# Kernel tuning notes

Hardware: AMD Instinct MI355X
Metric: run time of the kernel (lower is better)

Reference implementation:

```python
import jax, jax.numpy as jnp
from jax import lax
import numpy as np

B, T, F = 256, 2048, 12
EV_VOCAB, RS_VOCAB = 32, 8
EED, RED = 6, 3
H, K = 96, 3
D = F + EED + RED  # 21


def setup_inputs() -> dict:
    key = jax.random.key(0)
    ks = jax.random.split(key, 12)
    s = 0.05
    return {
        'seq': jax.random.normal(ks[0], (B, T, F), jnp.float32),
        'ev': jax.random.randint(ks[1], (B, T), 0, EV_VOCAB),
        'rs': jax.random.randint(ks[2], (B, T), 0, RS_VOCAB),
        'lengths': jax.random.randint(ks[3], (B,), 1, T + 1),  # valid lengths in [1, T]
        'event_emb': jax.random.normal(ks[4], (EV_VOCAB, EED), jnp.float32) * s,
        'result_emb': jax.random.normal(ks[5], (RS_VOCAB, RED), jnp.float32) * s,
        'W_ih': jax.random.normal(ks[6], (4 * H, D), jnp.float32) * s,
        'W_hh': jax.random.normal(ks[7], (4 * H, H), jnp.float32) * s,
        'b_ih': jnp.zeros((4 * H,), jnp.float32),
        'b_hh': jnp.zeros((4 * H,), jnp.float32),
        'W_mlp': jax.random.normal(ks[8], (H, H * K), jnp.float32) * s,
        'b_mlp': jnp.zeros((H,), jnp.float32),
        'W_fc': jax.random.normal(ks[9], (2, 2 * H), jnp.float32) * s,
        'b_fc': jnp.zeros((2,), jnp.float32),
    }


def reference(seq, ev, rs, lengths, event_emb, result_emb, W_ih, W_hh, b_ih, b_hh,
              W_mlp, b_mlp, W_fc, b_fc):
    # embed + concat -> [B,T,D]
    x = jnp.concatenate([seq, event_emb[ev], result_emb[rs]], axis=-1)
    xs = jnp.swapaxes(x, 0, 1)  # [T,B,D]
    ts = jnp.arange(T)
    b = b_ih + b_hh

    def step(carry, inp):
        h, c = carry
        x_t, t = inp
        gates = x_t @ W_ih.T + h @ W_hh.T + b  # [B,4H]
        i, f, g, o = jnp.split(gates, 4, axis=-1)  # PyTorch gate order i,f,g,o
        i = jax.nn.sigmoid(i); f = jax.nn.sigmoid(f)
        g = jnp.tanh(g); o = jax.nn.sigmoid(o)
        c_new = f * c + i * g
        h_new = o * jnp.tanh(c_new)
        m = (t < lengths)[:, None]  # packed-seq semantics: freeze state past length
        h = jnp.where(m, h_new, h)
        c = jnp.where(m, c_new, c)
        out = jnp.where(m, h_new, jnp.zeros_like(h_new))  # pad_packed zeros
        return (h, c), out

    h0 = jnp.zeros((B, H), x.dtype)
    (h_fin, _), outs = lax.scan(step, (h0, h0), (xs, ts))
    out_padded = jnp.swapaxes(outs, 0, 1)  # [B,T,H]

    # vectorized last-k gather (replaces torch Python loop)
    idx = lengths[:, None] - K + jnp.arange(K)  # [B,K]
    valid = idx >= 0
    gathered = jnp.take_along_axis(out_padded, jnp.clip(idx, 0)[:, :, None], axis=1)
    gathered = jnp.where(valid[:, :, None], gathered, jnp.zeros_like(gathered))
    lastk = gathered.reshape(B, K * H)

    h_lastk = jax.nn.relu(lastk @ W_mlp.T + b_mlp)
    h = jnp.concatenate([h_fin, h_lastk], axis=1)  # [B,2H]
    return h @ W_fc.T + b_fc  # [B,2]
```

## Files before the change

kernel.cpp:

```cpp
#include <hip/hip_runtime.h>

#define TT 2048
#define FF 12
#define HH 96
#define CH 128
#define L2E 1.44269504088896340736f

__device__ __forceinline__ float fast_exp2(float x){ return __builtin_amdgcn_exp2f(x); }
__device__ __forceinline__ float fast_rcp(float x){ return __builtin_amdgcn_rcpf(x); }

__global__ __launch_bounds__(512, 2) void lstm_persist(
  const float* __restrict__ seq, const int* __restrict__ ev, const int* __restrict__ rsi,
  const int* __restrict__ len, const float* __restrict__ eemb, const float* __restrict__ remb,
  const float* __restrict__ W_ih, const float* __restrict__ W_hh,
  const float* __restrict__ b_ih, const float* __restrict__ b_hh,
  const float* __restrict__ W_mlp, const float* __restrict__ b_mlp,
  const float* __restrict__ W_fc, const float* __restrict__ b_fc,
  float* __restrict__ out)
{
  const int b   = blockIdx.x;
  const int tid = threadIdx.x;
  const int w   = tid >> 6;
  const int l   = tid & 63;

  __shared__ __align__(16) float vh[HH];
  __shared__ __align__(16) float xch[CH][32];
  __shared__ __align__(16) float part[6*8*64];
  __shared__ __align__(16) float act[384];
  __shared__ __align__(16) float lastk[3*HH];
  __shared__ __align__(16) float h2[2*HH];
  __shared__ __align__(16) float et[32*6];
  __shared__ __align__(16) float rt[8*3];
  __shared__ int evb[CH];
  __shared__ int rsb[CH];

  float wreg[96];
  if (w < 6) {
    #pragma unroll
    for (int k = 0; k < 6; ++k) {
      const int g = l + 64*k;
      const float* p = W_hh + g*96 + 16*w;
      #pragma unroll
      for (int i = 0; i < 16; ++i) wreg[k*16+i] = p[i];
    }
  } else if (w == 6) {
    #pragma unroll
    for (int k = 0; k < 6; ++k) {
      const int g = l + 64*k;
      const float* p = W_ih + g*21;
      #pragma unroll
      for (int i = 0; i < 16; ++i) wreg[k*16+i] = p[i];
    }
  } else {
    #pragma unroll
    for (int k = 0; k < 6; ++k) {
      const int g = l + 64*k;
      #pragma unroll
      for (int i = 0; i < 16; ++i) {
        const int c = 16 + i;
        wreg[k*16+i] = (c < 21) ? W_ih[g*21 + c] : 0.f;
      }
    }
  }
  const float bg = (tid < 384) ? (b_ih[tid] + b_hh[tid]) : 0.f;

  for (int i = tid; i < HH;   i += 512) vh[i] = 0.f;
  for (int i = tid; i < 3*HH; i += 512) lastk[i] = 0.f;
  for (int i = tid; i < 192;  i += 512) et[i] = eemb[i];
  for (int i = tid; i < 24;   i += 512) rt[i] = remb[i];

  float c_state = 0.f;
  const int L = len[b];

  for (int t0 = 0; t0 < L; t0 += CH) {
    for (int q = tid; q < CH*FF; q += 512) {
      const int r = q / 12;
      const int c = q - r*12;
      xch[r][c] = seq[(size_t)b*(TT*FF) + (size_t)t0*FF + q];
    }
    if (tid < CH) {
      evb[tid] = ev [b*TT + t0 + tid];
      rsb[tid] = rsi[b*TT + t0 + tid];
    }
    __syncthreads();
    for (int q = tid; q < CH*20; q += 512) {
      const int r  = q / 20;
      const int cc = q - r*20 + 12;
      float val;
      if (cc < 18)      val = et[evb[r]*6 + (cc-12)];
      else if (cc < 21) val = rt[rsb[r]*3 + (cc-18)];
      else              val = 0.f;
      xch[r][cc] = val;
    }
    __syncthreads();

    const int nr = min(CH, L - t0);
    for (int r = 0; r < nr; ++r) {
      const float* sp = (w < 6) ? (vh + 16*w) : (&xch[r][16*(w-6)]);
      const float4 q0 = ((const float4*)sp)[0];
      const float4 q1 = ((const float4*)sp)[1];
      const float4 q2 = ((const float4*)sp)[2];
      const float4 q3 = ((const float4*)sp)[3];
      const float xv[16] = {q0.x,q0.y,q0.z,q0.w, q1.x,q1.y,q1.z,q1.w,
                            q2.x,q2.y,q2.z,q2.w, q3.x,q3.y,q3.z,q3.w};
      #pragma unroll
      for (int k = 0; k < 6; ++k) {
        float a = 0.f;
        #pragma unroll
        for (int i = 0; i < 16; ++i) a = fmaf(wreg[k*16+i], xv[i], a);
        part[(k*8 + w)*64 + l] = a;
      }
      __syncthreads();
      if (tid < 384) {
        float s = bg;
        const int kk = tid >> 6;
        const int ll = tid & 63;
        #pragma unroll
        for (int ww = 0; ww < 8; ++ww) s += part[(kk*8 + ww)*64 + ll];
        const bool is_t = (tid >= 192) && (tid < 288);
        const float arg = is_t ? (-2.f*L2E)*fabsf(s) : (-L2E)*s;
        const float e  = fast_exp2(arg);
        const float r1 = fast_rcp(1.f + e);
        const float th = copysignf((1.f - e) * r1, s);
        act[tid] = is_t ? th : r1;
      }
      __syncthreads();
      if (tid < 96) {
        const float i_ = act[tid];
        const float f_ = act[96  + tid];
        const float g_ = act[192 + tid];
        const float o_ = act[288 + tid];
        c_state = fmaf(f_, c_state, i_*g_);
        const float e  = fast_exp2((-2.f*L2E)*fabsf(c_state));
        const float th = copysignf((1.f - e) * fast_rcp(1.f + e), c_state);
        const float hn = o_ * th;
        vh[tid] = hn;
        const int kk = (t0 + r) + 3 - L;
        if (kk >= 0) lastk[kk*96 + tid] = hn;
      }
      __syncthreads();
    }
  }

  if (tid < 192) {
    const int hh = tid / 96;
    const int m  = tid - hh*96;
    const float* wp = W_mlp + m*288 + hh*144;
    const float* xp = lastk + hh*144;
    float s = 0.f;
    #pragma unroll 8
    for (int i = 0; i < 144; ++i) s = fmaf(wp[i], xp[i], s);
    act[tid] = s;
  }
  __syncthreads();
  if (tid < 96) {
    const float hl = act[tid] + act[96+tid] + b_mlp[tid];
    h2[96 + tid] = fmaxf(hl, 0.f);
    h2[tid] = vh[tid];
  }
  __syncthreads();
  if (tid < 128) {
    const int o  = tid >> 6;
    const int ll = tid & 63;
    const float* wf = W_fc + o*192 + 3*ll;
    float s = fmaf(wf[0], h2[3*ll+0], fmaf(wf[1], h2[3*ll+1], wf[2]*h2[3*ll+2]));
    #pragma unroll
    for (int off = 32; off > 0; off >>= 1) s += __shfl_down(s, off);
    if (ll == 0) out[b*2 + o] = s + b_fc[o];
  }
}

extern "C" void kernel_launch(void* const* d_in, const int* in_sizes, int n_in,
                              void* d_out, int out_size, void* d_ws, size_t ws_size,
                              hipStream_t stream) {
  const float* seq   = (const float*)d_in[0];
  const int*   ev    = (const int*)  d_in[1];
  const int*   rsi   = (const int*)  d_in[2];
  const int*   len   = (const int*)  d_in[3];
  const float* eemb  = (const float*)d_in[4];
  const float* remb  = (const float*)d_in[5];
  const float* W_ih  = (const float*)d_in[6];
  const float* W_hh  = (const float*)d_in[7];
  const float* b_ih  = (const float*)d_in[8];
  const float* b_hh  = (const float*)d_in[9];
  const float* W_mlp = (const float*)d_in[10];
  const float* b_mlp = (const float*)d_in[11];
  const float* W_fc  = (const float*)d_in[12];
  const float* b_fc  = (const float*)d_in[13];

  hipLaunchKernelGGL(lstm_persist, dim3(256), dim3(512), 0, stream,
                     seq, ev, rsi, len, eemb, remb, W_ih, W_hh, b_ih, b_hh,
                     W_mlp, b_mlp, W_fc, b_fc, (float*)d_out);
}
```

Baseline: 1.329 ms.

## Restructure LSTM step: per-thread gate rows, shuffle gate exchange, one barrier per step

Each of 384 threads now owns one full gate row, holding all of W_hh and W_ih in registers, so the cross-wave partial-sum reduction through shared memory goes away. The four gates of a hidden unit sit in adjacent lanes and are combined with xor shuffles. The hidden state is double-buffered, so each timestep needs one barrier instead of three. The input projection for the next step is computed ahead, and packed 2-wide FMAs are used for the recurrent dot product. The cost is much higher register pressure (about 117 weight registers per thread) and a serial 96-long dot product per thread on the critical path.

```diff
diff --git a/kernel.cpp b/kernel.cpp
--- a/kernel.cpp
+++ b/kernel.cpp
@@ -2,14 +2,17 @@
 
 #define TT 2048
 #define FF 12
-#define HH 96
 #define CH 128
 #define L2E 1.44269504088896340736f
 
+typedef float v2f __attribute__((ext_vector_type(2)));
+
 __device__ __forceinline__ float fast_exp2(float x){ return __builtin_amdgcn_exp2f(x); }
 __device__ __forceinline__ float fast_rcp(float x){ return __builtin_amdgcn_rcpf(x); }
+__device__ __forceinline__ v2f fma2(v2f a, v2f b, v2f c){ return __builtin_elementwise_fma(a, b, c); }
+__device__ __forceinline__ v2f mk2(float x, float y){ v2f r; r.x = x; r.y = y; return r; }
 
-__global__ __launch_bounds__(512, 2) void lstm_persist(
+__global__ __launch_bounds__(384, 2) void lstm_persist(
   const float* __restrict__ seq, const int* __restrict__ ev, const int* __restrict__ rsi,
   const int* __restrict__ len, const float* __restrict__ eemb, const float* __restrict__ remb,
   const float* __restrict__ W_ih, const float* __restrict__ W_hh,
@@ -20,143 +23,142 @@
 {
   const int b   = blockIdx.x;
   const int tid = threadIdx.x;
-  const int w   = tid >> 6;
-  const int l   = tid & 63;
+  const int qg  = tid & 3;
+  const int u   = tid >> 2;
+  const int g   = qg*96 + u;
 
-  __shared__ __align__(16) float vh[HH];
-  __shared__ __align__(16) float xch[CH][32];
-  __shared__ __align__(16) float part[6*8*64];
-  __shared__ __align__(16) float act[384];
-  __shared__ __align__(16) float lastk[3*HH];
-  __shared__ __align__(16) float h2[2*HH];
-  __shared__ __align__(16) float et[32*6];
-  __shared__ __align__(16) float rt[8*3];
+  __shared__ __align__(16) float xf[CH*24];
+  __shared__ __align__(16) float vhbuf[2*96];
+  __shared__ __align__(16) float lastk[3*96];
+  __shared__ __align__(16) float et[192];
+  __shared__ __align__(16) float rt[24];
+  __shared__ __align__(16) float accs[192];
+  __shared__ __align__(16) float h2[2*96];
   __shared__ int evb[CH];
   __shared__ int rsb[CH];
 
-  float wreg[96];
-  if (w < 6) {
+  v2f wh[48];
+  {
+    const float4* wp = (const float4*)(W_hh + g*96);
     #pragma unroll
-    for (int k = 0; k < 6; ++k) {
-      const int g = l + 64*k;
-      const float* p = W_hh + g*96 + 16*w;
-      #pragma unroll
-      for (int i = 0; i < 16; ++i) wreg[k*16+i] = p[i];
-    }
-  } else if (w == 6) {
-    #pragma unroll
-    for (int k = 0; k < 6; ++k) {
-      const int g = l + 64*k;
-      const float* p = W_ih + g*21;
-      #pragma unroll
-      for (int i = 0; i < 16; ++i) wreg[k*16+i] = p[i];
-    }
-  } else {
-    #pragma unroll
-    for (int k = 0; k < 6; ++k) {
-      const int g = l + 64*k;
-      #pragma unroll
-      for (int i = 0; i < 16; ++i) {
-        const int c = 16 + i;
-        wreg[k*16+i] = (c < 21) ? W_ih[g*21 + c] : 0.f;
-      }
+    for (int k = 0; k < 24; ++k) {
+      const float4 q4 = wp[k];
+      wh[2*k]   = mk2(q4.x, q4.y);
+      wh[2*k+1] = mk2(q4.z, q4.w);
     }
   }
-  const float bg = (tid < 384) ? (b_ih[tid] + b_hh[tid]) : 0.f;
+  float wi[21];
+  #pragma unroll
+  for (int c = 0; c < 21; ++c) wi[c] = W_ih[g*21 + c];
+  const float bg = b_ih[g] + b_hh[g];
 
-  for (int i = tid; i < HH;   i += 512) vh[i] = 0.f;
-  for (int i = tid; i < 3*HH; i += 512) lastk[i] = 0.f;
-  for (int i = tid; i < 192;  i += 512) et[i] = eemb[i];
-  for (int i = tid; i < 24;   i += 512) rt[i] = remb[i];
+  if (tid < 192) { vhbuf[tid] = 0.f; et[tid] = eemb[tid]; }
+  if (tid < 24)  rt[tid] = remb[tid];
+  if (tid < 288) lastk[tid] = 0.f;
 
   float c_state = 0.f;
   const int L = len[b];
 
   for (int t0 = 0; t0 < L; t0 += CH) {
-    for (int q = tid; q < CH*FF; q += 512) {
-      const int r = q / 12;
-      const int c = q - r*12;
-      xch[r][c] = seq[(size_t)b*(TT*FF) + (size_t)t0*FF + q];
+    #pragma unroll
+    for (int qq = 0; qq < 4; ++qq) {
+      const int i = tid + qq*384;
+      const int r = i/12, c = i - r*12;
+      xf[r*24 + c] = seq[(size_t)b*(TT*FF) + (size_t)t0*FF + i];
     }
     if (tid < CH) {
       evb[tid] = ev [b*TT + t0 + tid];
       rsb[tid] = rsi[b*TT + t0 + tid];
     }
     __syncthreads();
-    for (int q = tid; q < CH*20; q += 512) {
-      const int r  = q / 20;
-      const int cc = q - r*20 + 12;
-      float val;
-      if (cc < 18)      val = et[evb[r]*6 + (cc-12)];
-      else if (cc < 21) val = rt[rsb[r]*3 + (cc-18)];
-      else              val = 0.f;
-      xch[r][cc] = val;
+    #pragma unroll
+    for (int qq = 0; qq < 4; ++qq) {
+      const int i = tid + qq*384;
+      const int r = i/12, cc = i - r*12 + 12;
+      float v;
+      if (cc < 18)      v = et[evb[r]*6 + (cc-12)];
+      else if (cc < 21) v = rt[rsb[r]*3 + (cc-18)];
+      else              v = 0.f;
+      xf[r*24 + cc] = v;
     }
     __syncthreads();
 
     const int nr = min(CH, L - t0);
+    float xp;
+    {
+      const float* xr = xf;
+      float s0 = bg, s1 = 0.f, s2 = 0.f;
+      #pragma unroll
+      for (int c = 0; c < 7; ++c) {
+        s0 = fmaf(wi[c],    xr[c],    s0);
+        s1 = fmaf(wi[c+7],  xr[c+7],  s1);
+        s2 = fmaf(wi[c+14], xr[c+14], s2);
+      }
+      xp = s0 + s1 + s2;
+    }
+
     for (int r = 0; r < nr; ++r) {
-      const float* sp = (w < 6) ? (vh + 16*w) : (&xch[r][16*(w-6)]);
-      const float4 q0 = ((const float4*)sp)[0];
-      const float4 q1 = ((const float4*)sp)[1];
-      const float4 q2 = ((const float4*)sp)[2];
-      const float4 q3 = ((const float4*)sp)[3];
-      const float xv[16] = {q0.x,q0.y,q0.z,q0.w, q1.x,q1.y,q1.z,q1.w,
-                            q2.x,q2.y,q2.z,q2.w, q3.x,q3.y,q3.z,q3.w};
+      const float4* hq = (const float4*)(vhbuf + (r&1)*96);
+      v2f a0 = mk2(xp, 0.f), a1 = mk2(0.f,0.f), a2 = mk2(0.f,0.f), a3 = mk2(0.f,0.f);
       #pragma unroll
-      for (int k = 0; k < 6; ++k) {
-        float a = 0.f;
+      for (int k = 0; k < 24; k += 2) {
+        const float4 h4 = hq[k];
+        const float4 h5 = hq[k+1];
+        a0 = fma2(wh[2*k],   mk2(h4.x,h4.y), a0);
+        a1 = fma2(wh[2*k+1], mk2(h4.z,h4.w), a1);
+        a2 = fma2(wh[2*k+2], mk2(h5.x,h5.y), a2);
+        a3 = fma2(wh[2*k+3], mk2(h5.z,h5.w), a3);
+      }
+      const float s = ((a0.x+a0.y)+(a1.x+a1.y)) + ((a2.x+a2.y)+(a3.x+a3.y));
+      const bool is_t = (qg == 2);
+      const float arg = is_t ? (-2.f*L2E)*fabsf(s) : (-L2E)*s;
+      const float e  = fast_exp2(arg);
+      const float r1 = fast_rcp(1.f + e);
+      const float th = copysignf((1.f - e)*r1, s);
+      const float a  = is_t ? th : r1;
+      const float t1 = __shfl_xor(a, 2);
+      const float t2 = __shfl_xor(a, 1);
+      const float t3 = __shfl_xor(t1, 1);
+      if (qg == 0) {
+        c_state = fmaf(t2, c_state, a*t1);
+        const float e2  = fast_exp2((-2.f*L2E)*fabsf(c_state));
+        const float th2 = copysignf((1.f - e2)*fast_rcp(1.f + e2), c_state);
+        const float hn  = t3 * th2;
+        vhbuf[((r&1)^1)*96 + u] = hn;
+        const int kk = (t0 + r) + 3 - L;
+        if (kk >= 0) lastk[kk*96 + u] = hn;
+      }
+      if (r + 1 < nr) {
+        const float* xr = xf + (r+1)*24;
+        float s0 = bg, s1 = 0.f, s2 = 0.f;
         #pragma unroll
-        for (int i = 0; i < 16; ++i) a = fmaf(wreg[k*16+i], xv[i], a);
-        part[(k*8 + w)*64 + l] = a;
-      }
-      __syncthreads();
-      if (tid < 384) {
-        float s = bg;
-        const int kk = tid >> 6;
-        const int ll = tid & 63;
-        #pragma unroll
-        for (int ww = 0; ww < 8; ++ww) s += part[(kk*8 + ww)*64 + ll];
-        const bool is_t = (tid >= 192) && (tid < 288);
-        const float arg = is_t ? (-2.f*L2E)*fabsf(s) : (-L2E)*s;
-        const float e  = fast_exp2(arg);
-        const float r1 = fast_rcp(1.f + e);
-        const float th = copysignf((1.f - e) * r1, s);
-        act[tid] = is_t ? th : r1;
-      }
-      __syncthreads();
-      if (tid < 96) {
-        const float i_ = act[tid];
-        const float f_ = act[96  + tid];
-        const float g_ = act[192 + tid];
-        const float o_ = act[288 + tid];
-        c_state = fmaf(f_, c_state, i_*g_);
-        const float e  = fast_exp2((-2.f*L2E)*fabsf(c_state));
-        const float th = copysignf((1.f - e) * fast_rcp(1.f + e), c_state);
-        const float hn = o_ * th;
-        vh[tid] = hn;
-        const int kk = (t0 + r) + 3 - L;
-        if (kk >= 0) lastk[kk*96 + tid] = hn;
+        for (int c = 0; c < 7; ++c) {
+          s0 = fmaf(wi[c],    xr[c],    s0);
+          s1 = fmaf(wi[c+7],  xr[c+7],  s1);
+          s2 = fmaf(wi[c+14], xr[c+14], s2);
+        }
+        xp = s0 + s1 + s2;
       }
       __syncthreads();
     }
   }
 
+  const float* hf = vhbuf + (L & 1)*96;
   if (tid < 192) {
-    const int hh = tid / 96;
-    const int m  = tid - hh*96;
-    const float* wp = W_mlp + m*288 + hh*144;
-    const float* xp = lastk + hh*144;
+    const int half = tid / 96;
+    const int m    = tid - half*96;
+    const float* wp = W_mlp + m*288 + half*144;
+    const float* xq = lastk + half*144;
     float s = 0.f;
     #pragma unroll 8
-    for (int i = 0; i < 144; ++i) s = fmaf(wp[i], xp[i], s);
-    act[tid] = s;
+    for (int i = 0; i < 144; ++i) s = fmaf(wp[i], xq[i], s);
+    accs[tid] = s;
   }
   __syncthreads();
   if (tid < 96) {
-    const float hl = act[tid] + act[96+tid] + b_mlp[tid];
+    const float hl = accs[tid] + accs[96+tid] + b_mlp[tid];
     h2[96 + tid] = fmaxf(hl, 0.f);
-    h2[tid] = vh[tid];
+    h2[tid] = hf[tid];
   }
   __syncthreads();
   if (tid < 128) {
@@ -188,7 +190,7 @@
   const float* W_fc  = (const float*)d_in[12];
   const float* b_fc  = (const float*)d_in[13];
 
-  hipLaunchKernelGGL(lstm_persist, dim3(256), dim3(512), 0, stream,
+  hipLaunchKernelGGL(lstm_persist, dim3(256), dim3(384), 0, stream,
                      seq, ev, rsi, len, eemb, remb, W_ih, W_hh, b_ih, b_hh,
                      W_mlp, b_mlp, W_fc, b_fc, (float*)d_out);
 }
```

Measured after the change: 1.468 ms. 1.1x slower.

## Fuse gate activation and cell update via lane shuffles, use packed FMA

Applied to the files above, without the earlier changes.

Remaps the gate-reduction threads so each group of four adjacent lanes holds the i, f, g, o gates of one hidden unit. Shuffles then exchange the activations and the cell update runs in the same phase, which removes one block-wide barrier and the shared-memory act round trip per timestep. The per-step matvec now uses packed two-wide FMA on paired weight registers with split accumulators, and the partial-sum buffer is padded to a stride of 66. The cost is scattered reads of the partial sums and only a quarter of the lanes doing the cell update.

```diff
diff --git a/kernel.cpp b/kernel.cpp
--- a/kernel.cpp
+++ b/kernel.cpp
@@ -4,10 +4,15 @@
 #define FF 12
 #define HH 96
 #define CH 128
+#define PST 66
 #define L2E 1.44269504088896340736f
+
+typedef float v2f __attribute__((ext_vector_type(2)));
 
 __device__ __forceinline__ float fast_exp2(float x){ return __builtin_amdgcn_exp2f(x); }
 __device__ __forceinline__ float fast_rcp(float x){ return __builtin_amdgcn_rcpf(x); }
+__device__ __forceinline__ v2f fma2(v2f a, v2f b, v2f c){ return __builtin_elementwise_fma(a, b, c); }
+__device__ __forceinline__ v2f mk2(float x, float y){ v2f r; r.x = x; r.y = y; return r; }
 
 __global__ __launch_bounds__(512, 2) void lstm_persist(
   const float* __restrict__ seq, const int* __restrict__ ev, const int* __restrict__ rsi,
@@ -25,23 +30,23 @@
 
   __shared__ __align__(16) float vh[HH];
   __shared__ __align__(16) float xch[CH][32];
-  __shared__ __align__(16) float part[6*8*64];
-  __shared__ __align__(16) float act[384];
+  __shared__ __align__(16) float part[6*8*PST];
   __shared__ __align__(16) float lastk[3*HH];
   __shared__ __align__(16) float h2[2*HH];
+  __shared__ __align__(16) float accs[192];
   __shared__ __align__(16) float et[32*6];
   __shared__ __align__(16) float rt[8*3];
   __shared__ int evb[CH];
   __shared__ int rsb[CH];
 
-  float wreg[96];
+  v2f wreg[48];
   if (w < 6) {
     #pragma unroll
     for (int k = 0; k < 6; ++k) {
       const int g = l + 64*k;
       const float* p = W_hh + g*96 + 16*w;
       #pragma unroll
-      for (int i = 0; i < 16; ++i) wreg[k*16+i] = p[i];
+      for (int i = 0; i < 8; ++i) wreg[k*8+i] = mk2(p[2*i], p[2*i+1]);
     }
   } else if (w == 6) {
     #pragma unroll
@@ -49,20 +54,28 @@
       const int g = l + 64*k;
       const float* p = W_ih + g*21;
       #pragma unroll
-      for (int i = 0; i < 16; ++i) wreg[k*16+i] = p[i];
+      for (int i = 0; i < 8; ++i) wreg[k*8+i] = mk2(p[2*i], p[2*i+1]);
     }
   } else {
     #pragma unroll
     for (int k = 0; k < 6; ++k) {
       const int g = l + 64*k;
       #pragma unroll
-      for (int i = 0; i < 16; ++i) {
-        const int c = 16 + i;
-        wreg[k*16+i] = (c < 21) ? W_ih[g*21 + c] : 0.f;
+      for (int i = 0; i < 8; ++i) {
+        const int c0 = 16 + 2*i, c1 = 17 + 2*i;
+        const float w0 = (c0 < 21) ? W_ih[g*21 + c0] : 0.f;
+        const float w1 = (c1 < 21) ? W_ih[g*21 + c1] : 0.f;
+        wreg[k*8+i] = mk2(w0, w1);
       }
     }
   }
-  const float bg = (tid < 384) ? (b_ih[tid] + b_hh[tid]) : 0.f;
+
+  const int ub = tid >> 2;
+  const int qb = tid & 3;
+  const int gb = qb*96 + ub;
+  const float bg = (tid < 384) ? (b_ih[gb] + b_hh[gb]) : 0.f;
+  const int pk_ = gb >> 6;
+  const int pl_ = gb & 63;
 
   for (int i = tid; i < HH;   i += 512) vh[i] = 0.f;
   for (int i = tid; i < 3*HH; i += 512) lastk[i] = 0.f;
@@ -101,42 +114,47 @@
       const float4 q1 = ((const float4*)sp)[1];
       const float4 q2 = ((const float4*)sp)[2];
       const float4 q3 = ((const float4*)sp)[3];
-      const float xv[16] = {q0.x,q0.y,q0.z,q0.w, q1.x,q1.y,q1.z,q1.w,
-                            q2.x,q2.y,q2.z,q2.w, q3.x,q3.y,q3.z,q3.w};
+      v2f xv[8];
+      xv[0] = mk2(q0.x,q0.y); xv[1] = mk2(q0.z,q0.w);
+      xv[2] = mk2(q1.x,q1.y); xv[3] = mk2(q1.z,q1.w);
+      xv[4] = mk2(q2.x,q2.y); xv[5] = mk2(q2.z,q2.w);
+      xv[6] = mk2(q3.x,q3.y); xv[7] = mk2(q3.z,q3.w);
       #pragma unroll
       for (int k = 0; k < 6; ++k) {
-        float a = 0.f;
-        #pragma unroll
-        for (int i = 0; i < 16; ++i) a = fmaf(wreg[k*16+i], xv[i], a);
-        part[(k*8 + w)*64 + l] = a;
+        v2f a0 = mk2(0.f,0.f), a1 = mk2(0.f,0.f), a2 = mk2(0.f,0.f), a3 = mk2(0.f,0.f);
+        a0 = fma2(wreg[k*8+0], xv[0], a0);
+        a1 = fma2(wreg[k*8+1], xv[1], a1);
+        a2 = fma2(wreg[k*8+2], xv[2], a2);
+        a3 = fma2(wreg[k*8+3], xv[3], a3);
+        a0 = fma2(wreg[k*8+4], xv[4], a0);
+        a1 = fma2(wreg[k*8+5], xv[5], a1);
+        a2 = fma2(wreg[k*8+6], xv[6], a2);
+        a3 = fma2(wreg[k*8+7], xv[7], a3);
+        const v2f as = (a0 + a1) + (a2 + a3);
+        part[(k*8 + w)*PST + l] = as.x + as.y;
       }
       __syncthreads();
       if (tid < 384) {
         float s = bg;
-        const int kk = tid >> 6;
-        const int ll = tid & 63;
         #pragma unroll
-        for (int ww = 0; ww < 8; ++ww) s += part[(kk*8 + ww)*64 + ll];
-        const bool is_t = (tid >= 192) && (tid < 288);
+        for (int ww = 0; ww < 8; ++ww) s += part[(pk_*8 + ww)*PST + pl_];
+        const bool is_t = (qb == 2);
         const float arg = is_t ? (-2.f*L2E)*fabsf(s) : (-L2E)*s;
         const float e  = fast_exp2(arg);
         const float r1 = fast_rcp(1.f + e);
-        const float th = copysignf((1.f - e) * r1, s);
-        act[tid] = is_t ? th : r1;
-      }
-      __syncthreads();
-      if (tid < 96) {
-        const float i_ = act[tid];
-        const float f_ = act[96  + tid];
-        const float g_ = act[192 + tid];
-        const float o_ = act[288 + tid];
-        c_state = fmaf(f_, c_state, i_*g_);
-        const float e  = fast_exp2((-2.f*L2E)*fabsf(c_state));
-        const float th = copysignf((1.f - e) * fast_rcp(1.f + e), c_state);
-        const float hn = o_ * th;
-        vh[tid] = hn;
-        const int kk = (t0 + r) + 3 - L;
-        if (kk >= 0) lastk[kk*96 + tid] = hn;
+        const float a  = is_t ? copysignf((1.f - e)*r1, s) : r1;
+        const float t1 = __shfl_xor(a, 1);
+        const float t2 = __shfl_xor(a, 2);
+        const float t3 = __shfl_xor(a, 3);
+        if (qb == 0) {
+          c_state = fmaf(t1, c_state, a * t2);
+          const float e2 = fast_exp2((-2.f*L2E)*fabsf(c_state));
+          const float th = copysignf((1.f - e2)*fast_rcp(1.f + e2), c_state);
+          const float hn = t3 * th;
+          vh[ub] = hn;
+          const int kk = (t0 + r) + 3 - L;
+          if (kk >= 0) lastk[kk*96 + ub] = hn;
+        }
       }
       __syncthreads();
     }
@@ -150,11 +168,11 @@
     float s = 0.f;
     #pragma unroll 8
     for (int i = 0; i < 144; ++i) s = fmaf(wp[i], xp[i], s);
-    act[tid] = s;
+    accs[tid] = s;
   }
   __syncthreads();
   if (tid < 96) {
-    const float hl = act[tid] + act[96+tid] + b_mlp[tid];
+    const float hl = accs[tid] + accs[96+tid] + b_mlp[tid];
     h2[96 + tid] = fmaxf(hl, 0.f);
     h2[tid] = vh[tid];
   }
```

New measurement: 1.479 ms. 1.11x slower.

## Remap LSTM step to 16-lane groups with DPP reductions and one barrier

Applied to the files above, without the earlier changes.

Each 16-lane group now owns three hidden units' twelve gate rows. Four lanes split the combined h/x dot product and reduce it with quad DPP swaps, and the i/f/g/o activations are routed to the cell lanes with row-shift DPP. This removes the LDS partial-sum buffer and the separate activation pass, cutting the per-timestep barriers from three to one. h is double-buffered in shared memory so a single sync is safe. In exchange the lane-routing logic is intricate, and only 96 of 512 lanes do the cell update.

```diff
diff --git a/kernel.cpp b/kernel.cpp
--- a/kernel.cpp
+++ b/kernel.cpp
@@ -8,6 +8,13 @@
 
 __device__ __forceinline__ float fast_exp2(float x){ return __builtin_amdgcn_exp2f(x); }
 __device__ __forceinline__ float fast_rcp(float x){ return __builtin_amdgcn_rcpf(x); }
+
+#define DPPF(x, ctrl) __int_as_float(__builtin_amdgcn_update_dpp(0, __float_as_int(x), (ctrl), 0xF, 0xF, true))
+#define QP_XOR1 0xB1
+#define QP_XOR2 0x4E
+#define SHL4    0x104
+#define SHL8    0x108
+#define SHL12   0x10C
 
 __global__ __launch_bounds__(512, 2) void lstm_persist(
   const float* __restrict__ seq, const int* __restrict__ ev, const int* __restrict__ rsi,
@@ -20,51 +27,45 @@
 {
   const int b   = blockIdx.x;
   const int tid = threadIdx.x;
-  const int w   = tid >> 6;
-  const int l   = tid & 63;
-
-  __shared__ __align__(16) float vh[HH];
+  const int G   = tid >> 4;
+  const int lu  = tid & 15;
+  const int q   = lu >> 2;
+  const int c4  = lu & 3;
+
+  __shared__ __align__(16) float vv[2][128];
   __shared__ __align__(16) float xch[CH][32];
-  __shared__ __align__(16) float part[6*8*64];
-  __shared__ __align__(16) float act[384];
   __shared__ __align__(16) float lastk[3*HH];
-  __shared__ __align__(16) float h2[2*HH];
   __shared__ __align__(16) float et[32*6];
   __shared__ __align__(16) float rt[8*3];
+  __shared__ __align__(16) float accs[192];
+  __shared__ __align__(16) float h2[2*HH];
   __shared__ int evb[CH];
   __shared__ int rsb[CH];
 
-  float wreg[96];
-  if (w < 6) {
+  float wh[3][24];
+  float wx[3][6];
+  float bg[3];
+  bool  isT[3];
+  #pragma unroll
+  for (int j = 0; j < 3; ++j) {
+    const int rp = 12*G + 3*q + j;
+    const int u_ = rp >> 2;
+    const int qg = rp & 3;
+    const int grow = qg*96 + u_;
+    const float* ph = W_hh + grow*96 + 24*c4;
     #pragma unroll
-    for (int k = 0; k < 6; ++k) {
-      const int g = l + 64*k;
-      const float* p = W_hh + g*96 + 16*w;
-      #pragma unroll
-      for (int i = 0; i < 16; ++i) wreg[k*16+i] = p[i];
-    }
-  } else if (w == 6) {
+    for (int i = 0; i < 24; ++i) wh[j][i] = ph[i];
     #pragma unroll
-    for (int k = 0; k < 6; ++k) {
-      const int g = l + 64*k;
-      const float* p = W_ih + g*21;
-      #pragma unroll
-      for (int i = 0; i < 16; ++i) wreg[k*16+i] = p[i];
-    }
-  } else {
-    #pragma unroll
-    for (int k = 0; k < 6; ++k) {
-      const int g = l + 64*k;
-      #pragma unroll
-      for (int i = 0; i < 16; ++i) {
-        const int c = 16 + i;
-        wreg[k*16+i] = (c < 21) ? W_ih[g*21 + c] : 0.f;
-      }
-    }
-  }
-  const float bg = (tid < 384) ? (b_ih[tid] + b_hh[tid]) : 0.f;
-
-  for (int i = tid; i < HH;   i += 512) vh[i] = 0.f;
+    for (int i = 0; i < 6; ++i) {
+      const int cc = 6*c4 + i;
+      wx[j][i] = (cc < 21) ? W_ih[grow*21 + cc] : 0.f;
+    }
+    bg[j]  = (c4 == 0) ? (b_ih[grow] + b_hh[grow]) : 0.f;
+    isT[j] = (qg == 2);
+  }
+  const int un = 3*G + lu;
+
+  if (tid < 256) ((float*)vv)[tid] = 0.f;
   for (int i = tid; i < 3*HH; i += 512) lastk[i] = 0.f;
   for (int i = tid; i < 192;  i += 512) et[i] = eemb[i];
   for (int i = tid; i < 24;   i += 512) rt[i] = remb[i];
@@ -73,19 +74,19 @@
   const int L = len[b];
 
   for (int t0 = 0; t0 < L; t0 += CH) {
-    for (int q = tid; q < CH*FF; q += 512) {
-      const int r = q / 12;
-      const int c = q - r*12;
-      xch[r][c] = seq[(size_t)b*(TT*FF) + (size_t)t0*FF + q];
+    for (int i = tid; i < CH*FF; i += 512) {
+      const int r = i / 12;
+      const int c = i - r*12;
+      xch[r][c] = seq[(size_t)b*(TT*FF) + (size_t)t0*FF + i];
     }
     if (tid < CH) {
       evb[tid] = ev [b*TT + t0 + tid];
       rsb[tid] = rsi[b*TT + t0 + tid];
     }
     __syncthreads();
-    for (int q = tid; q < CH*20; q += 512) {
-      const int r  = q / 20;
-      const int cc = q - r*20 + 12;
+    for (int i = tid; i < CH*20; i += 512) {
+      const int r  = i / 20;
+      const int cc = i - r*20 + 12;
       float val;
       if (cc < 18)      val = et[evb[r]*6 + (cc-12)];
       else if (cc < 21) val = rt[rsb[r]*3 + (cc-18)];
@@ -96,67 +97,88 @@
 
     const int nr = min(CH, L - t0);
     for (int r = 0; r < nr; ++r) {
-      const float* sp = (w < 6) ? (vh + 16*w) : (&xch[r][16*(w-6)]);
-      const float4 q0 = ((const float4*)sp)[0];
-      const float4 q1 = ((const float4*)sp)[1];
-      const float4 q2 = ((const float4*)sp)[2];
-      const float4 q3 = ((const float4*)sp)[3];
-      const float xv[16] = {q0.x,q0.y,q0.z,q0.w, q1.x,q1.y,q1.z,q1.w,
-                            q2.x,q2.y,q2.z,q2.w, q3.x,q3.y,q3.z,q3.w};
-      #pragma unroll
-      for (int k = 0; k < 6; ++k) {
-        float a = 0.f;
+      const int p = (t0 + r) & 1;
+      const float* hp = vv[p] + 24*c4;
+      float hb[24];
+      #pragma unroll
+      for (int i = 0; i < 6; ++i) *(float4*)&hb[4*i] = ((const float4*)hp)[i];
+      const float* xp = &xch[r][6*c4];
+      float xb[6];
+      #pragma unroll
+      for (int i = 0; i < 3; ++i) *(float2*)&xb[2*i] = ((const float2*)xp)[i];
+
+      float S[3];
+      #pragma unroll
+      for (int j = 0; j < 3; ++j) {
+        float a0 = bg[j], a1 = 0.f, a2 = 0.f;
         #pragma unroll
-        for (int i = 0; i < 16; ++i) a = fmaf(wreg[k*16+i], xv[i], a);
-        part[(k*8 + w)*64 + l] = a;
+        for (int i = 0; i < 8; ++i) {
+          a0 = fmaf(wh[j][3*i+0], hb[3*i+0], a0);
+          a1 = fmaf(wh[j][3*i+1], hb[3*i+1], a1);
+          a2 = fmaf(wh[j][3*i+2], hb[3*i+2], a2);
+        }
+        a0 = fmaf(wx[j][0], xb[0], a0);
+        a1 = fmaf(wx[j][1], xb[1], a1);
+        a2 = fmaf(wx[j][2], xb[2], a2);
+        a0 = fmaf(wx[j][3], xb[3], a0);
+        a1 = fmaf(wx[j][4], xb[4], a1);
+        a2 = fmaf(wx[j][5], xb[5], a2);
+        float s = (a0 + a1) + a2;
+        s += DPPF(s, QP_XOR1);
+        s += DPPF(s, QP_XOR2);
+        S[j] = s;
+      }
+      float A[3];
+      #pragma unroll
+      for (int j = 0; j < 3; ++j) {
+        const float s = S[j];
+        const float arg = isT[j] ? (-2.f*L2E)*fabsf(s) : (-L2E)*s;
+        const float e  = fast_exp2(arg);
+        const float r1 = fast_rcp(1.f + e);
+        A[j] = isT[j] ? copysignf((1.f - e)*r1, s) : r1;
+      }
+      const float m1 = DPPF(A[0], SHL4);
+      const float m2 = DPPF(A[1], SHL4);
+      const float m3 = DPPF(A[2], SHL4);
+      const float m4 = DPPF(m1,  SHL4);
+      const float m5 = DPPF(m2,  SHL4);
+      const float s8 = DPPF(A[2], SHL8);
+      const float w9 = DPPF(A[0], SHL12);
+      const float wa = DPPF(A[1], SHL12);
+      const float wb = DPPF(A[2], SHL12);
+      if (lu < 3) {
+        const float il = (lu==0) ? A[0] : ((lu==1) ? m2 : s8);
+        const float fl = (lu==0) ? A[1] : ((lu==1) ? m3 : w9);
+        const float gl = (lu==0) ? A[2] : ((lu==1) ? m4 : wa);
+        const float ol = (lu==0) ? m1   : ((lu==1) ? m5 : wb);
+        c_state = fmaf(fl, c_state, il*gl);
+        const float e2 = fast_exp2((-2.f*L2E)*fabsf(c_state));
+        const float th = copysignf((1.f - e2)*fast_rcp(1.f + e2), c_state);
+        const float hn = ol * th;
+        vv[p^1][un] = hn;
+        const int kk = (t0 + r) + 3 - L;
+        if (kk >= 0) lastk[kk*96 + un] = hn;
       }
       __syncthreads();
-      if (tid < 384) {
-        float s = bg;
-        const int kk = tid >> 6;
-        const int ll = tid & 63;
-        #pragma unroll
-        for (int ww = 0; ww < 8; ++ww) s += part[(kk*8 + ww)*64 + ll];
-        const bool is_t = (tid >= 192) && (tid < 288);
-        const float arg = is_t ? (-2.f*L2E)*fabsf(s) : (-L2E)*s;
-        const float e  = fast_exp2(arg);
-        const float r1 = fast_rcp(1.f + e);
-        const float th = copysignf((1.f - e) * r1, s);
-        act[tid] = is_t ? th : r1;
-      }
-      __syncthreads();
-      if (tid < 96) {
-        const float i_ = act[tid];
-        const float f_ = act[96  + tid];
-        const float g_ = act[192 + tid];
-        const float o_ = act[288 + tid];
-        c_state = fmaf(f_, c_state, i_*g_);
-        const float e  = fast_exp2((-2.f*L2E)*fabsf(c_state));
-        const float th = copysignf((1.f - e) * fast_rcp(1.f + e), c_state);
-        const float hn = o_ * th;
-        vh[tid] = hn;
-        const int kk = (t0 + r) + 3 - L;
-        if (kk >= 0) lastk[kk*96 + tid] = hn;
-      }
-      __syncthreads();
-    }
-  }
-
+    }
+  }
+
+  const float* hfin = vv[L & 1];
   if (tid < 192) {
     const int hh = tid / 96;
     const int m  = tid - hh*96;
     const float* wp = W_mlp + m*288 + hh*144;
-    const float* xp = lastk + hh*144;
+    const float* xq = lastk + hh*144;
     float s = 0.f;
     #pragma unroll 8
-    for (int i = 0; i < 144; ++i) s = fmaf(wp[i], xp[i], s);
-    act[tid] = s;
+    for (int i = 0; i < 144; ++i) s = fmaf(wp[i], xq[i], s);
+    accs[tid] = s;
   }
   __syncthreads();
   if (tid < 96) {
-    const float hl = act[tid] + act[96+tid] + b_mlp[tid];
+    const float hl = accs[tid] + accs[96+tid] + b_mlp[tid];
     h2[96 + tid] = fmaxf(hl, 0.f);
-    h2[tid] = vh[tid];
+    h2[tid] = hfin[tid];
   }
   __syncthreads();
   if (tid < 128) {
```

New measurement: 1.367 ms. +2.8%, slower.
